# Performance work log

Measured on AMD Instinct MI355X. Metric: run time of the kernel, lower is better.

Reference implementation:

```python
import jax, jax.numpy as jnp
import numpy as np

NQ = 4  # qubits
silu = jax.nn.silu


def _ry(t):
    c, s = jnp.cos(t / 2), jnp.sin(t / 2)
    return jnp.stack([jnp.stack([c, -s]), jnp.stack([s, c])]).astype(jnp.complex64)


def _rz(t):
    e = jnp.exp(-0.5j * t.astype(jnp.complex64))
    z = jnp.zeros((), jnp.complex64)
    return jnp.stack([jnp.stack([e, z]), jnp.stack([z, jnp.conj(e)])])


def _ap1(state, U, w):
    # apply 2x2 unitary U on wire w of a (2,)*NQ statevector
    s = jnp.tensordot(U, jnp.moveaxis(state, w, 0), axes=1)
    return jnp.moveaxis(s, 0, w)


def _cnot(state, c, t):
    s = jnp.moveaxis(state, (c, t), (0, 1))
    s = jnp.stack([s[0], s[1, ::-1]], axis=0)
    return jnp.moveaxis(s, (0, 1), (c, t))


def _circuit(inp, w):
    # batched 4-qubit state-vector simulation of the PennyLane qnode
    state = jnp.zeros((2,) * NQ, jnp.complex64).at[(0,) * NQ].set(1.0)
    for i in range(NQ):
        state = _ap1(state, _ry(inp[i]), i)
    for i in range(NQ):
        state = _ap1(state, _rz(w[i, 0]), i)
        state = _ap1(state, _ry(w[i, 1]), i)
    for i in range(NQ - 1):
        state = _cnot(state, i, i + 1)
    for i in range(NQ):
        state = _ap1(state, _rz(w[i + NQ, 0]), i)
        state = _ap1(state, _ry(w[i + NQ, 1]), i)
    p = state.real ** 2 + state.imag ** 2
    sign = jnp.array([1.0, -1.0], p.dtype)
    return jnp.stack([jnp.tensordot(p, sign, axes=[[i], [0]]).sum() for i in range(NQ)])


def _bn(x, p, eps=1e-5):
    # p: [4, C] = (gamma, beta, running_mean, running_var); eval-mode batchnorm
    g, b, m, v = p
    shp = (1, -1) + (1,) * (x.ndim - 2)
    return (x - m.reshape(shp)) * (g.reshape(shp) / jnp.sqrt(v.reshape(shp) + eps)) + b.reshape(shp)


def _conv(x, w, b, pad, dil=1):
    y = jax.lax.conv_general_dilated(x, w, (1,), [(pad, pad)], rhs_dilation=(dil,),
                                     dimension_numbers=('NCH', 'OIH', 'NCH'))
    return y + b[None, :, None]


def _forward(x, W1, b1, bn1, Wa1, ba1, bna1, Wa2, ba2, bna2,
             Wd1, bd1, bnd1, Wd2, bd2, bnd2, Wr1, br1, bnr1, Wr2, br2, bnr2,
             Wfm, bfm, qw, Wf1, bf1, bnf1, Wf2, bf2, bnf2, Wf3, bf3):
    h = silu(_bn(_conv(x, W1, b1, 2), bn1))                    # [B,64,L]
    a = silu(_bn(_conv(h, Wa1, ba1, 3), bna1))                 # [B,32,L]
    a = jax.nn.sigmoid(_bn(_conv(a, Wa2, ba2, 3), bna2))       # [B,64,L]
    h = h * a
    h = silu(_bn(_conv(h, Wd1, bd1, 2, 2), bnd1))              # [B,128,L]
    h = silu(_bn(_conv(h, Wd2, bd2, 4, 4), bnd2))              # [B,128,L]
    idn = h
    r = silu(_bn(_conv(h, Wr1, br1, 1), bnr1))
    r = _bn(_conv(r, Wr2, br2, 1), bnr2)                       # (dropout is identity in eval)
    h = silu(r + idn)
    g = h.mean(axis=2)                                         # global avg pool -> [B,128]
    qin = g @ Wfm.T + bfm                                      # feature map -> [B,4]
    q = jax.vmap(_circuit, in_axes=(0, None))(qin, qw)         # [B,4]
    x1 = silu(_bn(q @ Wf1.T + bf1, bnf1))
    x2 = silu(_bn(x1 @ Wf2.T + bf2, bnf2))
    return x2 @ Wf3.T + bf3                                    # [B,1]


def setup_inputs() -> dict:
    key = jax.random.key(0)
    ks = iter(jax.random.split(key, 64))

    def w(*shape, scale=0.05):
        return jax.random.normal(next(ks), shape, jnp.float32) * scale

    def bnp(c):
        g = 1.0 + 0.1 * jax.random.normal(next(ks), (c,), jnp.float32)
        b = 0.1 * jax.random.normal(next(ks), (c,), jnp.float32)
        m = 0.1 * jax.random.normal(next(ks), (c,), jnp.float32)
        v = 1.0 + 0.1 * jax.random.uniform(next(ks), (c,), jnp.float32)
        return jnp.stack([g, b, m, v])

    B, L = 128, 4096
    return dict(
        x=jax.random.normal(next(ks), (B, 1, L), jnp.float32),
        W1=w(64, 1, 5), b1=w(64), bn1=bnp(64),
        Wa1=w(32, 64, 7), ba1=w(32), bna1=bnp(32),
        Wa2=w(64, 32, 7), ba2=w(64), bna2=bnp(64),
        Wd1=w(128, 64, 3), bd1=w(128), bnd1=bnp(128),
        Wd2=w(128, 128, 3), bd2=w(128), bnd2=bnp(128),
        Wr1=w(128, 128, 3), br1=w(128), bnr1=bnp(128),
        Wr2=w(128, 128, 3), br2=w(128), bnr2=bnp(128),
        Wfm=w(4, 128), bfm=w(4),
        qw=jax.random.uniform(next(ks), (8, 2), jnp.float32, 0.0, 2 * np.pi),
        Wf1=w(64, 4, scale=0.2), bf1=w(64), bnf1=bnp(64),
        Wf2=w(32, 64, scale=0.2), bf2=w(32), bnf2=bnp(32),
        Wf3=w(1, 32, scale=0.2), bf3=w(1),
    )


def reference(x, W1, b1, bn1, Wa1, ba1, bna1, Wa2, ba2, bna2,
              Wd1, bd1, bnd1, Wd2, bd2, bnd2, Wr1, br1, bnr1, Wr2, br2, bnr2,
              Wfm, bfm, qw, Wf1, bf1, bnf1, Wf2, bf2, bnf2, Wf3, bf3):
    return _forward(x, W1, b1, bn1, Wa1, ba1, bna1, Wa2, ba2, bna2,
                    Wd1, bd1, bnd1, Wd2, bd2, bnd2, Wr1, br1, bnr1, Wr2, br2, bnr2,
                    Wfm, bfm, qw, Wf1, bf1, bnf1, Wf2, bf2, bnf2, Wf3, bf3)
```

## Files before the change

kernel.cpp:

```cpp
#include <hip/hip_runtime.h>
#include <math.h>

#define L_LEN 4096
#define DEV __device__ __forceinline__

typedef __attribute__((ext_vector_type(8))) _Float16 f16x8;
typedef __attribute__((ext_vector_type(4))) float   f32x4;

DEV float fexp_f(float x) { return exp2f(1.44269504f * x); }
DEV float silu_f(float x) { return x * __builtin_amdgcn_rcpf(1.f + fexp_f(-x)); }
DEV float sigm_f(float x) { return __builtin_amdgcn_rcpf(1.f + fexp_f(-x)); }

DEV void gload16(const void* g, void* l) {
    __builtin_amdgcn_global_load_lds(
        (const __attribute__((address_space(1))) void*)g,
        (__attribute__((address_space(3))) void*)l, 16, 0, 0);
}

__global__ __launch_bounds__(256) void conv1_k(
    const float* __restrict__ x, const float* __restrict__ W,
    const float* __restrict__ bias, const float* __restrict__ bnp,
    _Float16* __restrict__ out)
{
    __shared__ float sw[64 * 5];
    __shared__ float ssc[64], ssh[64];
    const int tid = threadIdx.x;
    if (tid < 64) {
        float g = bnp[tid], be = bnp[64 + tid], mn = bnp[128 + tid], vr = bnp[192 + tid];
        float sc = g * rsqrtf(vr + 1e-5f);
        ssc[tid] = sc;
        ssh[tid] = fmaf(bias[tid] - mn, sc, be);
    }
    for (int i = tid; i < 320; i += 256) sw[i] = W[i];
    __syncthreads();

    const int b = blockIdx.y;
    const int l = blockIdx.x * 64 + (tid >> 2);
    const int cq = (tid & 3) * 16;

    float win[5];
#pragma unroll
    for (int k = 0; k < 5; ++k) {
        int ix = l + k - 2;
        win[k] = (ix >= 0 && ix < L_LEN) ? x[(size_t)b * L_LEN + ix] : 0.f;
    }
    __align__(16) _Float16 vv[16];
#pragma unroll
    for (int j = 0; j < 16; ++j) {
        const int co = cq + j;
        float z = 0.f;
#pragma unroll
        for (int k = 0; k < 5; ++k) z = fmaf(sw[co * 5 + k], win[k], z);
        z = fmaf(z, ssc[co], ssh[co]);
        vv[j] = (_Float16)silu_f(z);
    }
    const size_t o = ((size_t)b * L_LEN + l) * 64 + cq;
    *(int4*)(out + o)     = *(const int4*)(vv);
    *(int4*)(out + o + 8) = *(const int4*)(vv + 8);
}

template <int CIN, int COUT, int K>
__global__ void prep_w_k(const float* __restrict__ W, _Float16* __restrict__ wf)
{
    constexpr int NTILE = COUT / 16;
    const int i = blockIdx.x * 256 + threadIdx.x;
    const int total = (CIN / 32) * K * NTILE * 64;
    if (i >= total) return;
    const int lane = i & 63;
    int r = i >> 6;
    const int n  = r % NTILE; r /= NTILE;
    const int t  = r % K;
    const int s  = r / K;

    const int co  = n * 16 + (lane & 15);
    const int cib = s * 32 + (lane >> 4) * 8;
    __align__(16) _Float16 v8[8];
#pragma unroll
    for (int j = 0; j < 8; ++j)
        v8[j] = (_Float16)W[((size_t)co * CIN + cib + j) * K + t];
    *(int4*)(wf + (size_t)i * 8) = *(const int4*)v8;
}

template <int CIN, int COUT, int K, int DIL, int MODE>
__launch_bounds__(256, 2) __global__ void conv_mfma_k(
    const _Float16* __restrict__ in, const _Float16* __restrict__ wf,
    const float* __restrict__ bias,  const float* __restrict__ bnp,
    const _Float16* __restrict__ aux, _Float16* __restrict__ out,
    float* __restrict__ gsum, const float* __restrict__ zpage)
{
    constexpr int SL    = CIN / 32;
    constexpr int P     = SL * K;
    constexpr int PADR  = ((K - 1) / 2) * DIL;
    constexpr int LWIN  = 128 + (K - 1) * DIL;
    constexpr int NT    = COUT / 32;
    constexpr int NTILE = COUT / 16;
    constexpr int SLOTS = CIN / 8 + 1;
    constexpr int RSTR  = SLOTS * 16;
    constexpr int CH_IN = LWIN * SLOTS;
    constexpr int STGB  = LWIN * RSTR;
    constexpr int ESTR  = COUT + 4;
    constexpr int EPIB  = 128 * ESTR * 2;
    constexpr int SMEMB = (STGB > EPIB) ? STGB : EPIB;

    __shared__ __align__(16) char smem[SMEMB];
    __shared__ float pf[(MODE == 3) ? 4 : 1][COUT];

    const int tid   = threadIdx.x;
    const int lane  = tid & 63;
    const int w     = tid >> 6;
    const int wl    = w >> 1;
    const int wc    = w & 1;
    const int b     = blockIdx.z;
    const int l0    = blockIdx.x * 128;
    const int lan15 = lane & 15;
    const int kgB   = (lane >> 4) * 16;

    const size_t bL = (size_t)b * L_LEN;

    auto loadB = [&](int p, f16x8 (&dst)[NT]) {
        const _Float16* bbase = wf + (size_t)p * (NTILE * 512);
#pragma unroll
        for (int nt = 0; nt < NT; ++nt) {
            const int ntg = wc * NT + nt;
            dst[nt] = *(const f16x8*)(bbase + ntg * 512 + lane * 8);
        }
    };

    f32x4 acc[4][NT];
#pragma unroll
    for (int mt = 0; mt < 4; ++mt)
#pragma unroll
        for (int nt = 0; nt < NT; ++nt) acc[mt][nt] = (f32x4){0.f, 0.f, 0.f, 0.f};

    f16x8 brbuf[2][NT];

    for (int c = tid; c < CH_IN; c += 256) {
        const int row  = c / SLOTS;
        const int slot = c - row * SLOTS;
        const int gl   = l0 - PADR + row;
        const bool ok  = (slot < SLOTS - 1) & (gl >= 0) & (gl < L_LEN);
        const _Float16* s0 = in + ((bL + gl) * CIN + slot * 8);
        const void* src = ok ? (const void*)s0 : (const void*)zpage;
        gload16(src, smem + (size_t)c * 16);
    }
    loadB(0, brbuf[0]);
    if (P > 1) loadB(1, brbuf[1]);
    asm volatile("s_waitcnt vmcnt(0)" ::: "memory");
    __builtin_amdgcn_sched_barrier(0);
    __syncthreads();

#pragma unroll
    for (int pp = 0; pp < P; ++pp) {
        const int ss = pp / K;
        const int tt = pp % K;
#pragma unroll
        for (int mt = 0; mt < 4; ++mt) {
            const int row = wl * 64 + mt * 16 + lan15 + tt * DIL;
            const f16x8 a = *(const f16x8*)(smem + row * RSTR + ss * 64 + kgB);
#pragma unroll
            for (int nt = 0; nt < NT; ++nt) {
                acc[mt][nt] = __builtin_amdgcn_mfma_f32_16x16x32_f16(brbuf[pp & 1][nt], a, acc[mt][nt], 0, 0, 0);
            }
        }
        if (pp + 2 < P) loadB(pp + 2, brbuf[pp & 1]);
    }

    __syncthreads();
    _Float16* zl = (_Float16*)smem;
#pragma unroll
    for (int nt = 0; nt < NT; ++nt) {
        const int co0 = (wc * NT + nt) * 16 + (lane >> 4) * 4;
        const float4 g4 = *(const float4*)&bnp[co0];
        const float4 b4 = *(const float4*)&bnp[COUT + co0];
        const float4 m4 = *(const float4*)&bnp[2 * COUT + co0];
        const float4 v4 = *(const float4*)&bnp[3 * COUT + co0];
        const float4 bi = *(const float4*)&bias[co0];
        float sc[4], sh[4];
        sc[0] = g4.x * rsqrtf(v4.x + 1e-5f); sh[0] = fmaf(bi.x - m4.x, sc[0], b4.x);
        sc[1] = g4.y * rsqrtf(v4.y + 1e-5f); sh[1] = fmaf(bi.y - m4.y, sc[1], b4.y);
        sc[2] = g4.z * rsqrtf(v4.z + 1e-5f); sh[2] = fmaf(bi.z - m4.z, sc[2], b4.z);
        sc[3] = g4.w * rsqrtf(v4.w + 1e-5f); sh[3] = fmaf(bi.w - m4.w, sc[3], b4.w);
#pragma unroll
        for (int mt = 0; mt < 4; ++mt) {
            const int l_loc = wl * 64 + mt * 16 + lan15;
            __align__(8) _Float16 h4[4];
#pragma unroll
            for (int r = 0; r < 4; ++r)
                h4[r] = (_Float16)fmaf(acc[mt][nt][r], sc[r], sh[r]);
            *(int2*)&zl[l_loc * ESTR + co0] = *(const int2*)h4;
        }
    }
    __syncthreads();

    constexpr int CO8 = COUT / 8;
    constexpr int LG  = (CO8 == 16) ? 4 : (CO8 == 8) ? 3 : 2;
    constexpr int RPI = 64 / CO8;
    const int co = (lane & (CO8 - 1)) * 8;

    float ps[8];
#pragma unroll
    for (int j = 0; j < 8; ++j) ps[j] = 0.f;

#pragma unroll
    for (int s2 = 0; s2 < CO8 / 2; ++s2) {
        const int l = w * 32 + s2 * RPI + (lane >> LG);
        _Float16 z8[8];
        *(int4*)z8 = *(const int4*)&zl[l * ESTR + co];
        const size_t gidx = (bL + l0 + l) * COUT + co;
        if constexpr (MODE == 0) {
            __align__(16) _Float16 o8[8];
#pragma unroll
            for (int j = 0; j < 8; ++j) o8[j] = (_Float16)silu_f((float)z8[j]);
            *(int4*)(out + gidx) = *(const int4*)o8;
        } else if constexpr (MODE == 1) {
            _Float16 g8[8];
            *(int4*)g8 = *(const int4*)(aux + gidx);
            __align__(16) _Float16 o8[8];
#pragma unroll
            for (int j = 0; j < 8; ++j) o8[j] = (_Float16)((float)g8[j] * sigm_f((float)z8[j]));
            *(int4*)(out + gidx) = *(const int4*)o8;
        } else {
            _Float16 a8[8];
            *(int4*)a8 = *(const int4*)(aux + gidx);
#pragma unroll
            for (int j = 0; j < 8; ++j) ps[j] += silu_f((float)z8[j] + (float)a8[j]);
        }
    }

    if constexpr (MODE == 3) {
#pragma unroll
        for (int j = 0; j < 8; ++j) {
#pragma unroll
            for (int m = CO8; m < 64; m <<= 1)
                ps[j] += __shfl_xor(ps[j], m, 64);
        }
        if (lane < CO8) {
#pragma unroll
            for (int j = 0; j < 8; ++j) pf[w][co + j] = ps[j];
        }
        __syncthreads();
        if (tid < COUT) {
            const float s = pf[0][tid] + pf[1][tid] + pf[2][tid] + pf[3][tid];
            atomicAdd(&gsum[b * COUT + tid], s);
        }
    }
}

template <int BW> DEV void g_ry(float (&re)[16], float (&im)[16], float t) {
    float s, c; sincosf(0.5f * t, &s, &c);
#pragma unroll
    for (int i = 0; i < 16; ++i)
        if (!(i & BW)) {
            const int j = i | BW;
            float r0 = re[i], q0 = im[i], r1 = re[j], q1 = im[j];
            re[i] = c * r0 - s * r1; im[i] = c * q0 - s * q1;
            re[j] = s * r0 + c * r1; im[j] = s * q0 + c * q1;
        }
}
template <int BW> DEV void g_rz(float (&re)[16], float (&im)[16], float t) {
    float s, c; sincosf(0.5f * t, &s, &c);
#pragma unroll
    for (int i = 0; i < 16; ++i) {
        float r = re[i], q = im[i];
        if (i & BW) { re[i] = r * c - q * s; im[i] = q * c + r * s; }
        else        { re[i] = r * c + q * s; im[i] = q * c - r * s; }
    }
}
template <int BC, int BT> DEV void g_cnot(float (&re)[16], float (&im)[16]) {
#pragma unroll
    for (int i = 0; i < 16; ++i)
        if ((i & BC) && !(i & BT)) {
            const int j = i | BT;
            float r = re[i]; re[i] = re[j]; re[j] = r;
            float q = im[i]; im[i] = im[j]; im[j] = q;
        }
}

__global__ void quantum_k(const float* __restrict__ gsum, const float* __restrict__ Wfm,
                          const float* __restrict__ bfm, const float* __restrict__ qw,
                          float* __restrict__ q, int B)
{
    const int b = blockIdx.x * blockDim.x + threadIdx.x;
    if (b >= B) return;

    float qin[4];
#pragma unroll
    for (int j = 0; j < 4; ++j) qin[j] = bfm[j];
    const float inv = 1.f / (float)L_LEN;
    for (int c = 0; c < 128; ++c) {
        const float gv = gsum[b * 128 + c] * inv;
#pragma unroll
        for (int j = 0; j < 4; ++j) qin[j] = fmaf(gv, Wfm[j * 128 + c], qin[j]);
    }

    float re[16], im[16];
#pragma unroll
    for (int i = 0; i < 16; ++i) { re[i] = 0.f; im[i] = 0.f; }
    re[0] = 1.f;

    g_ry<8>(re, im, qin[0]); g_ry<4>(re, im, qin[1]); g_ry<2>(re, im, qin[2]); g_ry<1>(re, im, qin[3]);
    g_rz<8>(re, im, qw[0]);  g_ry<8>(re, im, qw[1]);
    g_rz<4>(re, im, qw[2]);  g_ry<4>(re, im, qw[3]);
    g_rz<2>(re, im, qw[4]);  g_ry<2>(re, im, qw[5]);
    g_rz<1>(re, im, qw[6]);  g_ry<1>(re, im, qw[7]);
    g_cnot<8, 4>(re, im); g_cnot<4, 2>(re, im); g_cnot<2, 1>(re, im);
    g_rz<8>(re, im, qw[8]);  g_ry<8>(re, im, qw[9]);
    g_rz<4>(re, im, qw[10]); g_ry<4>(re, im, qw[11]);
    g_rz<2>(re, im, qw[12]); g_ry<2>(re, im, qw[13]);
    g_rz<1>(re, im, qw[14]); g_ry<1>(re, im, qw[15]);

    float pr[16];
#pragma unroll
    for (int i = 0; i < 16; ++i) pr[i] = re[i] * re[i] + im[i] * im[i];
#pragma unroll
    for (int w = 0; w < 4; ++w) {
        const int bw = 8 >> w;
        float e = 0.f;
#pragma unroll
        for (int i = 0; i < 16; ++i) e += (i & bw) ? -pr[i] : pr[i];
        q[b * 4 + w] = e;
    }
}

__global__ void head_k(const float* __restrict__ q,
                       const float* __restrict__ Wf1, const float* __restrict__ bf1, const float* __restrict__ bnf1,
                       const float* __restrict__ Wf2, const float* __restrict__ bf2, const float* __restrict__ bnf2,
                       const float* __restrict__ Wf3, const float* __restrict__ bf3,
                       float* __restrict__ out)
{
    const int b = blockIdx.x, t = threadIdx.x;
    __shared__ float qs[4], x1[64], x2[32];
    if (t < 4) qs[t] = q[b * 4 + t];
    __syncthreads();
    {
        float a = bf1[t];
#pragma unroll
        for (int k = 0; k < 4; ++k) a = fmaf(qs[k], Wf1[t * 4 + k], a);
        const float sc = bnf1[t] / sqrtf(bnf1[192 + t] + 1e-5f);
        const float z  = (a - bnf1[128 + t]) * sc + bnf1[64 + t];
        x1[t] = silu_f(z);
    }
    __syncthreads();
    if (t < 32) {
        float a = bf2[t];
        for (int k = 0; k < 64; ++k) a = fmaf(x1[k], Wf2[t * 64 + k], a);
        const float sc = bnf2[t] / sqrtf(bnf2[96 + t] + 1e-5f);
        const float z  = (a - bnf2[64 + t]) * sc + bnf2[32 + t];
        x2[t] = silu_f(z);
    }
    __syncthreads();
    if (t == 0) {
        float a = bf3[0];
        for (int k = 0; k < 32; ++k) a = fmaf(x2[k], Wf3[k], a);
        out[b] = a;
    }
}

extern "C" void kernel_launch(void* const* d_in, const int* in_sizes, int n_in,
                              void* d_out, int out_size, void* d_ws, size_t ws_size,
                              hipStream_t stream)
{
    (void)n_in; (void)out_size;
    const float* x    = (const float*)d_in[0];
    const float* W1   = (const float*)d_in[1];
    const float* b1   = (const float*)d_in[2];
    const float* bn1  = (const float*)d_in[3];
    const float* Wa1  = (const float*)d_in[4];
    const float* ba1  = (const float*)d_in[5];
    const float* bna1 = (const float*)d_in[6];
    const float* Wa2  = (const float*)d_in[7];
    const float* ba2  = (const float*)d_in[8];
    const float* bna2 = (const float*)d_in[9];
    const float* Wd1  = (const float*)d_in[10];
    const float* bdd1 = (const float*)d_in[11];
    const float* bnd1 = (const float*)d_in[12];
    const float* Wd2  = (const float*)d_in[13];
    const float* bdd2 = (const float*)d_in[14];
    const float* bnd2 = (const float*)d_in[15];
    const float* Wr1  = (const float*)d_in[16];
    const float* br1  = (const float*)d_in[17];
    const float* bnr1 = (const float*)d_in[18];
    const float* Wr2  = (const float*)d_in[19];
    const float* br2  = (const float*)d_in[20];
    const float* bnr2 = (const float*)d_in[21];
    const float* Wfm  = (const float*)d_in[22];
    const float* bfm  = (const float*)d_in[23];
    const float* qw   = (const float*)d_in[24];
    const float* Wf1  = (const float*)d_in[25];
    const float* bf1  = (const float*)d_in[26];
    const float* bnf1 = (const float*)d_in[27];
    const float* Wf2  = (const float*)d_in[28];
    const float* bf2  = (const float*)d_in[29];
    const float* bnf2 = (const float*)d_in[30];
    const float* Wf3  = (const float*)d_in[31];
    const float* bf3  = (const float*)d_in[32];

    const int B = in_sizes[0] / L_LEN;

    char* base = (char*)d_ws;
    size_t off = 0;
    auto alloc = [&](size_t bytes) -> char* {
        off = (off + 255) & ~(size_t)255;
        char* p = base + off;
        off += bytes;
        return p;
    };

    float* gbuf  = (float*)alloc((size_t)B * 128 * 4);
    float* qbuf  = (float*)alloc((size_t)B * 4 * 4);
    float* zpage = (float*)alloc(256);

    auto wfrag = [&](int cin, int cout, int k) -> _Float16* {
        return (_Float16*)alloc((size_t)k * cout * cin * 2);
    };
    _Float16* wa1f = wfrag(64, 32, 7);
    _Float16* wa2f = wfrag(32, 64, 7);
    _Float16* wd1f = wfrag(64, 128, 3);
    _Float16* wd2f = wfrag(128, 128, 3);
    _Float16* wr1f = wfrag(128, 128, 3);
    _Float16* wr2f = wfrag(128, 128, 3);

    const size_t fixed = (off + 255) & ~(size_t)255;
    const size_t PS = (size_t)2 * L_LEN * (64 + 32 + 128 + 128);
    size_t avail = (ws_size > fixed + 4096) ? ws_size - fixed - 4096 : 0;
    int chunk = B;
    while (chunk > 1 && (size_t)chunk * PS > avail) chunk >>= 1;

    auto aplane = [&](int C, int c) -> _Float16* {
        return (_Float16*)alloc((size_t)c * L_LEN * C * 2);
    };
    _Float16* h0 = aplane(64,  chunk);
    _Float16* a1 = aplane(32,  chunk);
    _Float16* d1 = aplane(128, chunk);
    _Float16* d2 = aplane(128, chunk);
    _Float16* r1 = d1;

    auto pg = [](int tot) { return dim3((tot + 255) / 256); };
    prep_w_k<64, 32, 7>  <<<pg(2*7*2*64),  dim3(256), 0, stream>>>(Wa1, wa1f);
    prep_w_k<32, 64, 7>  <<<pg(1*7*4*64),  dim3(256), 0, stream>>>(Wa2, wa2f);
    prep_w_k<64, 128, 3> <<<pg(2*3*8*64),  dim3(256), 0, stream>>>(Wd1, wd1f);
    prep_w_k<128, 128, 3><<<pg(4*3*8*64),  dim3(256), 0, stream>>>(Wd2, wd2f);
    prep_w_k<128, 128, 3><<<pg(4*3*8*64),  dim3(256), 0, stream>>>(Wr1, wr1f);
    prep_w_k<128, 128, 3><<<pg(4*3*8*64),  dim3(256), 0, stream>>>(Wr2, wr2f);

    hipMemsetAsync(gbuf, 0, (size_t)B * 128 * sizeof(float), stream);
    hipMemsetAsync(zpage, 0, 256, stream);

    const dim3 blk(256);
    for (int sft = 0; sft < B; sft += chunk) {
        const int c = (chunk < B - sft) ? chunk : (B - sft);
        const dim3 cg(L_LEN / 128, 1, c);
        conv1_k<<<dim3(64, c), blk, 0, stream>>>(x + (size_t)sft * L_LEN, W1, b1, bn1, h0);
        conv_mfma_k<64, 32, 7, 1, 0><<<cg, blk, 0, stream>>>(h0, wa1f, ba1, bna1, nullptr, a1, nullptr, zpage);
        conv_mfma_k<32, 64, 7, 1, 1><<<cg, blk, 0, stream>>>(a1, wa2f, ba2, bna2, h0, h0, nullptr, zpage);
        conv_mfma_k<64, 128, 3, 2, 0><<<cg, blk, 0, stream>>>(h0, wd1f, bdd1, bnd1, nullptr, d1, nullptr, zpage);
        conv_mfma_k<128, 128, 3, 4, 0><<<cg, blk, 0, stream>>>(d1, wd2f, bdd2, bnd2, nullptr, d2, nullptr, zpage);
        conv_mfma_k<128, 128, 3, 1, 0><<<cg, blk, 0, stream>>>(d2, wr1f, br1, bnr1, nullptr, r1, nullptr, zpage);
        conv_mfma_k<128, 128, 3, 1, 3><<<cg, blk, 0, stream>>>(r1, wr2f, br2, bnr2, d2, nullptr, gbuf + (size_t)sft * 128, zpage);
    }

    quantum_k<<<dim3((B + 127) / 128), dim3(128), 0, stream>>>(gbuf, Wfm, bfm, qw, qbuf, B);
    head_k<<<dim3(B), dim3(64), 0, stream>>>(qbuf, Wf1, bf1, bnf1, Wf2, bf2, bnf2, Wf3, bf3, (float*)d_out);
}
```

Before: 467.9 us.

## Write conv epilogue directly from accumulators, merge weight prep and head kernels

Result: no change. 471.6 us (+0.8%).

```diff
diff --git a/kernel.cpp b/kernel.cpp
--- a/kernel.cpp
+++ b/kernel.cpp
@@ -59,26 +59,36 @@
     *(int4*)(out + o + 8) = *(const int4*)(vv + 8);
 }
 
-template <int CIN, int COUT, int K>
-__global__ void prep_w_k(const float* __restrict__ W, _Float16* __restrict__ wf)
+struct PrepArgs {
+    const float* W[6];
+    _Float16*    wf[6];
+    int cin[6], cout[6], kk[6];
+    int cum[7];
+};
+
+__global__ void prep_all_k(PrepArgs a)
 {
-    constexpr int NTILE = COUT / 16;
-    const int i = blockIdx.x * 256 + threadIdx.x;
-    const int total = (CIN / 32) * K * NTILE * 64;
-    if (i >= total) return;
-    const int lane = i & 63;
-    int r = i >> 6;
-    const int n  = r % NTILE; r /= NTILE;
-    const int t  = r % K;
-    const int s  = r / K;
+    const int id0 = blockIdx.x * 256 + threadIdx.x;
+    if (id0 >= a.cum[6]) return;
+    int sg = 0;
+    while (sg < 5 && id0 >= a.cum[sg + 1]) ++sg;
+    const int id   = id0 - a.cum[sg];
+    const int CIN  = a.cin[sg], COUT = a.cout[sg], K = a.kk[sg];
+    const int NTILE = COUT / 16;
+    const int lane = id & 63;
+    int r = id >> 6;
+    const int n = r % NTILE; r /= NTILE;
+    const int t = r % K;
+    const int s = r / K;
 
     const int co  = n * 16 + (lane & 15);
     const int cib = s * 32 + (lane >> 4) * 8;
+    const float* W = a.W[sg];
     __align__(16) _Float16 v8[8];
 #pragma unroll
     for (int j = 0; j < 8; ++j)
         v8[j] = (_Float16)W[((size_t)co * CIN + cib + j) * K + t];
-    *(int4*)(wf + (size_t)i * 8) = *(const int4*)v8;
+    *(int4*)(a.wf[sg] + (size_t)id * 8) = *(const int4*)v8;
 }
 
 template <int CIN, int COUT, int K, int DIL, int MODE>
@@ -97,13 +107,9 @@
     constexpr int SLOTS = CIN / 8 + 1;
     constexpr int RSTR  = SLOTS * 16;
     constexpr int CH_IN = LWIN * SLOTS;
-    constexpr int STGB  = LWIN * RSTR;
-    constexpr int ESTR  = COUT + 4;
-    constexpr int EPIB  = 128 * ESTR * 2;
-    constexpr int SMEMB = (STGB > EPIB) ? STGB : EPIB;
-
-    __shared__ __align__(16) char smem[SMEMB];
-    __shared__ float pf[(MODE == 3) ? 4 : 1][COUT];
+
+    __shared__ __align__(16) char smem[LWIN * RSTR];
+    __shared__ float pf[(MODE == 3) ? 2 : 1][COUT];
 
     const int tid   = threadIdx.x;
     const int lane  = tid & 63;
@@ -165,8 +171,6 @@
         if (pp + 2 < P) loadB(pp + 2, brbuf[pp & 1]);
     }
 
-    __syncthreads();
-    _Float16* zl = (_Float16*)smem;
 #pragma unroll
     for (int nt = 0; nt < NT; ++nt) {
         const int co0 = (wc * NT + nt) * 16 + (lane >> 4) * 4;
@@ -180,69 +184,54 @@
         sc[1] = g4.y * rsqrtf(v4.y + 1e-5f); sh[1] = fmaf(bi.y - m4.y, sc[1], b4.y);
         sc[2] = g4.z * rsqrtf(v4.z + 1e-5f); sh[2] = fmaf(bi.z - m4.z, sc[2], b4.z);
         sc[3] = g4.w * rsqrtf(v4.w + 1e-5f); sh[3] = fmaf(bi.w - m4.w, sc[3], b4.w);
+
+        float ps[4] = {0.f, 0.f, 0.f, 0.f};
 #pragma unroll
         for (int mt = 0; mt < 4; ++mt) {
-            const int l_loc = wl * 64 + mt * 16 + lan15;
-            __align__(8) _Float16 h4[4];
-#pragma unroll
-            for (int r = 0; r < 4; ++r)
-                h4[r] = (_Float16)fmaf(acc[mt][nt][r], sc[r], sh[r]);
-            *(int2*)&zl[l_loc * ESTR + co0] = *(const int2*)h4;
-        }
-    }
-    __syncthreads();
-
-    constexpr int CO8 = COUT / 8;
-    constexpr int LG  = (CO8 == 16) ? 4 : (CO8 == 8) ? 3 : 2;
-    constexpr int RPI = 64 / CO8;
-    const int co = (lane & (CO8 - 1)) * 8;
-
-    float ps[8];
-#pragma unroll
-    for (int j = 0; j < 8; ++j) ps[j] = 0.f;
-
-#pragma unroll
-    for (int s2 = 0; s2 < CO8 / 2; ++s2) {
-        const int l = w * 32 + s2 * RPI + (lane >> LG);
-        _Float16 z8[8];
-        *(int4*)z8 = *(const int4*)&zl[l * ESTR + co];
-        const size_t gidx = (bL + l0 + l) * COUT + co;
-        if constexpr (MODE == 0) {
-            __align__(16) _Float16 o8[8];
-#pragma unroll
-            for (int j = 0; j < 8; ++j) o8[j] = (_Float16)silu_f((float)z8[j]);
-            *(int4*)(out + gidx) = *(const int4*)o8;
-        } else if constexpr (MODE == 1) {
-            _Float16 g8[8];
-            *(int4*)g8 = *(const int4*)(aux + gidx);
-            __align__(16) _Float16 o8[8];
-#pragma unroll
-            for (int j = 0; j < 8; ++j) o8[j] = (_Float16)((float)g8[j] * sigm_f((float)z8[j]));
-            *(int4*)(out + gidx) = *(const int4*)o8;
-        } else {
-            _Float16 a8[8];
-            *(int4*)a8 = *(const int4*)(aux + gidx);
-#pragma unroll
-            for (int j = 0; j < 8; ++j) ps[j] += silu_f((float)z8[j] + (float)a8[j]);
+            const int l = wl * 64 + mt * 16 + lan15;
+            const size_t gi = (bL + l0 + l) * COUT + co0;
+            if constexpr (MODE == 0) {
+                __align__(8) _Float16 o4[4];
+#pragma unroll
+                for (int r = 0; r < 4; ++r)
+                    o4[r] = (_Float16)silu_f(fmaf(acc[mt][nt][r], sc[r], sh[r]));
+                *(int2*)(out + gi) = *(const int2*)o4;
+            } else if constexpr (MODE == 1) {
+                _Float16 g8[4];
+                *(int2*)g8 = *(const int2*)(aux + gi);
+                __align__(8) _Float16 o4[4];
+#pragma unroll
+                for (int r = 0; r < 4; ++r)
+                    o4[r] = (_Float16)((float)g8[r] * sigm_f(fmaf(acc[mt][nt][r], sc[r], sh[r])));
+                *(int2*)(out + gi) = *(const int2*)o4;
+            } else {
+                _Float16 a4[4];
+                *(int2*)a4 = *(const int2*)(aux + gi);
+#pragma unroll
+                for (int r = 0; r < 4; ++r)
+                    ps[r] += silu_f(fmaf(acc[mt][nt][r], sc[r], sh[r]) + (float)a4[r]);
+            }
+        }
+        if constexpr (MODE == 3) {
+#pragma unroll
+            for (int r = 0; r < 4; ++r) {
+                ps[r] += __shfl_xor(ps[r], 1, 64);
+                ps[r] += __shfl_xor(ps[r], 2, 64);
+                ps[r] += __shfl_xor(ps[r], 4, 64);
+                ps[r] += __shfl_xor(ps[r], 8, 64);
+            }
+            if (lan15 == 0) {
+#pragma unroll
+                for (int r = 0; r < 4; ++r)
+                    pf[wl][co0 + r] = ps[r];
+            }
         }
     }
 
     if constexpr (MODE == 3) {
-#pragma unroll
-        for (int j = 0; j < 8; ++j) {
-#pragma unroll
-            for (int m = CO8; m < 64; m <<= 1)
-                ps[j] += __shfl_xor(ps[j], m, 64);
-        }
-        if (lane < CO8) {
-#pragma unroll
-            for (int j = 0; j < 8; ++j) pf[w][co + j] = ps[j];
-        }
         __syncthreads();
-        if (tid < COUT) {
-            const float s = pf[0][tid] + pf[1][tid] + pf[2][tid] + pf[3][tid];
-            atomicAdd(&gsum[b * COUT + tid], s);
-        }
+        if (tid < COUT)
+            atomicAdd(&gsum[b * COUT + tid], pf[0][tid] + pf[1][tid]);
     }
 }
 
@@ -276,29 +265,38 @@
         }
 }
 
-__global__ void quantum_k(const float* __restrict__ gsum, const float* __restrict__ Wfm,
-                          const float* __restrict__ bfm, const float* __restrict__ qw,
-                          float* __restrict__ q, int B)
+__global__ __launch_bounds__(64) void qhead_k(
+    const float* __restrict__ gsum, const float* __restrict__ Wfm,
+    const float* __restrict__ bfm, const float* __restrict__ qw,
+    const float* __restrict__ Wf1, const float* __restrict__ bf1, const float* __restrict__ bnf1,
+    const float* __restrict__ Wf2, const float* __restrict__ bf2, const float* __restrict__ bnf2,
+    const float* __restrict__ Wf3, const float* __restrict__ bf3,
+    float* __restrict__ out)
 {
-    const int b = blockIdx.x * blockDim.x + threadIdx.x;
-    if (b >= B) return;
-
-    float qin[4];
-#pragma unroll
-    for (int j = 0; j < 4; ++j) qin[j] = bfm[j];
+    const int b = blockIdx.x, t = threadIdx.x;
     const float inv = 1.f / (float)L_LEN;
-    for (int c = 0; c < 128; ++c) {
-        const float gv = gsum[b * 128 + c] * inv;
-#pragma unroll
-        for (int j = 0; j < 4; ++j) qin[j] = fmaf(gv, Wfm[j * 128 + c], qin[j]);
+
+    float part[4];
+    {
+        const float gv0 = gsum[b * 128 + t] * inv;
+        const float gv1 = gsum[b * 128 + 64 + t] * inv;
+#pragma unroll
+        for (int j = 0; j < 4; ++j)
+            part[j] = gv0 * Wfm[j * 128 + t] + gv1 * Wfm[j * 128 + 64 + t];
+    }
+#pragma unroll
+    for (int j = 0; j < 4; ++j) {
+#pragma unroll
+        for (int m = 1; m < 64; m <<= 1)
+            part[j] += __shfl_xor(part[j], m, 64);
+        part[j] += bfm[j];
     }
 
     float re[16], im[16];
 #pragma unroll
     for (int i = 0; i < 16; ++i) { re[i] = 0.f; im[i] = 0.f; }
     re[0] = 1.f;
-
-    g_ry<8>(re, im, qin[0]); g_ry<4>(re, im, qin[1]); g_ry<2>(re, im, qin[2]); g_ry<1>(re, im, qin[3]);
+    g_ry<8>(re, im, part[0]); g_ry<4>(re, im, part[1]); g_ry<2>(re, im, part[2]); g_ry<1>(re, im, part[3]);
     g_rz<8>(re, im, qw[0]);  g_ry<8>(re, im, qw[1]);
     g_rz<4>(re, im, qw[2]);  g_ry<4>(re, im, qw[3]);
     g_rz<2>(re, im, qw[4]);  g_ry<2>(re, im, qw[5]);
@@ -312,30 +310,21 @@
     float pr[16];
 #pragma unroll
     for (int i = 0; i < 16; ++i) pr[i] = re[i] * re[i] + im[i] * im[i];
+    float q[4];
 #pragma unroll
     for (int w = 0; w < 4; ++w) {
         const int bw = 8 >> w;
         float e = 0.f;
 #pragma unroll
         for (int i = 0; i < 16; ++i) e += (i & bw) ? -pr[i] : pr[i];
-        q[b * 4 + w] = e;
-    }
-}
-
-__global__ void head_k(const float* __restrict__ q,
-                       const float* __restrict__ Wf1, const float* __restrict__ bf1, const float* __restrict__ bnf1,
-                       const float* __restrict__ Wf2, const float* __restrict__ bf2, const float* __restrict__ bnf2,
-                       const float* __restrict__ Wf3, const float* __restrict__ bf3,
-                       float* __restrict__ out)
-{
-    const int b = blockIdx.x, t = threadIdx.x;
-    __shared__ float qs[4], x1[64], x2[32];
-    if (t < 4) qs[t] = q[b * 4 + t];
-    __syncthreads();
+        q[w] = e;
+    }
+
+    __shared__ float x1[64], x2[32];
     {
         float a = bf1[t];
 #pragma unroll
-        for (int k = 0; k < 4; ++k) a = fmaf(qs[k], Wf1[t * 4 + k], a);
+        for (int k = 0; k < 4; ++k) a = fmaf(q[k], Wf1[t * 4 + k], a);
         const float sc = bnf1[t] / sqrtf(bnf1[192 + t] + 1e-5f);
         const float z  = (a - bnf1[128 + t]) * sc + bnf1[64 + t];
         x1[t] = silu_f(z);
@@ -407,7 +396,6 @@
     };
 
     float* gbuf  = (float*)alloc((size_t)B * 128 * 4);
-    float* qbuf  = (float*)alloc((size_t)B * 4 * 4);
     float* zpage = (float*)alloc(256);
 
     auto wfrag = [&](int cin, int cout, int k) -> _Float16* {
@@ -435,13 +423,17 @@
     _Float16* d2 = aplane(128, chunk);
     _Float16* r1 = d1;
 
-    auto pg = [](int tot) { return dim3((tot + 255) / 256); };
-    prep_w_k<64, 32, 7>  <<<pg(2*7*2*64),  dim3(256), 0, stream>>>(Wa1, wa1f);
-    prep_w_k<32, 64, 7>  <<<pg(1*7*4*64),  dim3(256), 0, stream>>>(Wa2, wa2f);
-    prep_w_k<64, 128, 3> <<<pg(2*3*8*64),  dim3(256), 0, stream>>>(Wd1, wd1f);
-    prep_w_k<128, 128, 3><<<pg(4*3*8*64),  dim3(256), 0, stream>>>(Wd2, wd2f);
-    prep_w_k<128, 128, 3><<<pg(4*3*8*64),  dim3(256), 0, stream>>>(Wr1, wr1f);
-    prep_w_k<128, 128, 3><<<pg(4*3*8*64),  dim3(256), 0, stream>>>(Wr2, wr2f);
+    PrepArgs pa;
+    pa.W[0] = Wa1; pa.wf[0] = wa1f; pa.cin[0] = 64;  pa.cout[0] = 32;  pa.kk[0] = 7;
+    pa.W[1] = Wa2; pa.wf[1] = wa2f; pa.cin[1] = 32;  pa.cout[1] = 64;  pa.kk[1] = 7;
+    pa.W[2] = Wd1; pa.wf[2] = wd1f; pa.cin[2] = 64;  pa.cout[2] = 128; pa.kk[2] = 3;
+    pa.W[3] = Wd2; pa.wf[3] = wd2f; pa.cin[3] = 128; pa.cout[3] = 128; pa.kk[3] = 3;
+    pa.W[4] = Wr1; pa.wf[4] = wr1f; pa.cin[4] = 128; pa.cout[4] = 128; pa.kk[4] = 3;
+    pa.W[5] = Wr2; pa.wf[5] = wr2f; pa.cin[5] = 128; pa.cout[5] = 128; pa.kk[5] = 3;
+    pa.cum[0] = 0;
+    for (int i = 0; i < 6; ++i)
+        pa.cum[i + 1] = pa.cum[i] + (pa.cin[i] / 32) * pa.kk[i] * (pa.cout[i] / 16) * 64;
+    prep_all_k<<<dim3((pa.cum[6] + 255) / 256), dim3(256), 0, stream>>>(pa);
 
     hipMemsetAsync(gbuf, 0, (size_t)B * 128 * sizeof(float), stream);
     hipMemsetAsync(zpage, 0, 256, stream);
@@ -459,6 +451,7 @@
         conv_mfma_k<128, 128, 3, 1, 3><<<cg, blk, 0, stream>>>(r1, wr2f, br2, bnr2, d2, nullptr, gbuf + (size_t)sft * 128, zpage);
     }
 
-    quantum_k<<<dim3((B + 127) / 128), dim3(128), 0, stream>>>(gbuf, Wfm, bfm, qw, qbuf, B);
-    head_k<<<dim3(B), dim3(64), 0, stream>>>(qbuf, Wf1, bf1, bnf1, Wf2, bf2, bnf2, Wf3, bf3, (float*)d_out);
-}
+    qhead_k<<<dim3(B), dim3(64), 0, stream>>>(gbuf, Wfm, bfm, qw,
+                                              Wf1, bf1, bnf1, Wf2, bf2, bnf2, Wf3, bf3,
+                                              (float*)d_out);
+}
```
